# Optimization experiments

Hardware: AMD Instinct MI355X
Metric: run time of the kernel (lower is better)

Reference implementation:

```python
import jax, jax.numpy as jnp
import numpy as np
import math

N_HEAD = 16
V_HEAD = 32   # v_head_dim
NOPE = 32     # nope_head_dim
ROPE_D = 64   # rope_head_dim
KEEP = 256    # num_tokens_to_keep
EPS = 1e-6


def _freqs(T, dim=ROPE_D, theta=10000.0):
    f = 1.0 / (theta ** (jnp.arange(0, dim, 2, dtype=jnp.float32) / dim))
    t = jnp.arange(T, dtype=jnp.float32)
    a = jnp.outer(t, f)  # [T, dim//2]
    return jnp.cos(a), jnp.sin(a)


def _rope(x, cos, sin):
    # x: [B,H,S,D]; half-split rotation as in apply_rope
    S = x.shape[-2]
    c = cos[:S][None, None]
    s = sin[:S][None, None]
    x1, x2 = jnp.split(x, 2, axis=-1)
    return jnp.concatenate([x1 * c - x2 * s, x1 * s + x2 * c], axis=-1)


def _rms(x, g, eps=EPS):
    return x * jax.lax.rsqrt(jnp.mean(x * x, axis=-1, keepdims=True) + eps) * g


def _attn(q, k, v, causal):
    scale = 1.0 / math.sqrt(q.shape[-1])
    s = jnp.einsum('bhqd,bhkd->bhqk', q, k) * scale
    if causal:
        Tq, Tk = s.shape[-2], s.shape[-1]
        mask = jnp.tril(jnp.ones((Tq, Tk), dtype=bool))
        s = jnp.where(mask, s, jnp.finfo(s.dtype).min)
    return jnp.einsum('bhqk,bhkd->bhqd', jax.nn.softmax(s, axis=-1), v)


def _forward(x, w_cq, g_qnorm, w_dq_nope, w_dq_rope, w_ckv, g_kvnorm,
             w_dk_nope, w_dv, w_krope, w_imp, w_selk, w_selv,
             w_wink, w_winv, w_gate, w_proj):
    B, T, C = x.shape
    cos, sin = _freqs(T)

    # --- MLA query path ---
    nq = _rms(x @ w_cq, g_qnorm)                                  # [B,T,96]
    q_nope = (nq @ w_dq_nope).reshape(B, T, N_HEAD, NOPE).transpose(0, 2, 1, 3)
    q_rope = (nq @ w_dq_rope).reshape(B, T, N_HEAD, ROPE_D).transpose(0, 2, 1, 3)
    q_rope = _rope(q_rope, cos, sin)
    q = jnp.concatenate([q_nope, q_rope], axis=-1)                # [B,H,T,96]

    # --- branch gate ---
    gate = jax.nn.softmax((x @ w_gate).mean(axis=1), axis=-1)     # [B,3]

    # --- branch 1: MLA-compressed full KV ---
    ckv = _rms(x @ w_ckv, g_kvnorm)                               # [B,T,32]
    k_nope = (ckv @ w_dk_nope).reshape(B, T, N_HEAD, NOPE).transpose(0, 2, 1, 3)
    v1 = (ckv @ w_dv).reshape(B, T, N_HEAD, V_HEAD).transpose(0, 2, 1, 3)
    k_rope = (x @ w_krope).reshape(B, T, 1, ROPE_D).transpose(0, 2, 1, 3) / N_HEAD
    k_rope = _rope(k_rope, cos, sin)
    k1 = jnp.concatenate(
        [k_nope, jnp.broadcast_to(k_rope, (B, N_HEAD, T, ROPE_D))], axis=-1)

    # --- branch 2: top-k selected tokens ---
    scores = (x @ w_imp)[..., 0]                                  # [B,T]
    _, idx = jax.lax.top_k(scores, KEEP)
    idx = jnp.sort(idx, axis=1)
    sel = jnp.take_along_axis(x, idx[:, :, None], axis=1)         # [B,S,C]
    ks = (sel @ w_selk).reshape(B, KEEP, N_HEAD, NOPE + ROPE_D).transpose(0, 2, 1, 3)
    vs = (sel @ w_selv).reshape(B, KEEP, N_HEAD, V_HEAD).transpose(0, 2, 1, 3)
    ks = jnp.concatenate([ks[..., :NOPE], _rope(ks[..., NOPE:], cos, sin)], axis=-1)

    # --- branch 3: sliding window (training mode -> full x) ---
    kw = (x @ w_wink).reshape(B, T, N_HEAD, NOPE + ROPE_D).transpose(0, 2, 1, 3)
    vw = (x @ w_winv).reshape(B, T, N_HEAD, V_HEAD).transpose(0, 2, 1, 3)
    kw = jnp.concatenate([kw[..., :NOPE], _rope(kw[..., NOPE:], cos, sin)], axis=-1)

    a1 = _attn(q, k1, v1, causal=True)
    a2 = _attn(q, ks, vs, causal=False)
    a3 = _attn(q, kw, vw, causal=True)

    g = gate[:, :, None, None, None]
    out = g[:, 0] * a1 + g[:, 1] * a2 + g[:, 2] * a3              # [B,H,T,Vd]
    out = out.transpose(0, 2, 1, 3).reshape(B, T, N_HEAD * V_HEAD)
    return out @ w_proj                                           # [B,T,C]


def setup_inputs() -> dict:
    key = jax.random.key(0)
    ks = jax.random.split(key, 20)
    B, T, C = 2, 1024, 1024
    q_lora, kv_lora = 96, 32
    std = 0.02
    def w(k, shape):
        return jax.random.normal(k, shape, dtype=jnp.float32) * std
    return {
        'x': jax.random.normal(ks[0], (B, T, C), dtype=jnp.float32),
        'w_cq': w(ks[1], (C, q_lora)),
        'g_qnorm': jnp.ones((q_lora,), jnp.float32),
        'w_dq_nope': w(ks[2], (q_lora, N_HEAD * NOPE)),
        'w_dq_rope': w(ks[3], (q_lora, N_HEAD * ROPE_D)),
        'w_ckv': w(ks[4], (C, kv_lora)),
        'g_kvnorm': jnp.ones((kv_lora,), jnp.float32),
        'w_dk_nope': w(ks[5], (kv_lora, N_HEAD * NOPE)),
        'w_dv': w(ks[6], (kv_lora, N_HEAD * V_HEAD)),
        'w_krope': w(ks[7], (C, ROPE_D)),
        'w_imp': w(ks[8], (C, 1)),
        'w_selk': w(ks[9], (C, N_HEAD * (NOPE + ROPE_D))),
        'w_selv': w(ks[10], (C, N_HEAD * V_HEAD)),
        'w_wink': w(ks[11], (C, N_HEAD * (NOPE + ROPE_D))),
        'w_winv': w(ks[12], (C, N_HEAD * V_HEAD)),
        'w_gate': w(ks[13], (C, 3)),
        'w_proj': w(ks[14], (N_HEAD * V_HEAD, C)),
    }


def reference(x, w_cq, g_qnorm, w_dq_nope, w_dq_rope, w_ckv, g_kvnorm,
              w_dk_nope, w_dv, w_krope, w_imp, w_selk, w_selv,
              w_wink, w_winv, w_gate, w_proj):
    return _forward(x, w_cq, g_qnorm, w_dq_nope, w_dq_rope, w_ckv, g_kvnorm,
                    w_dk_nope, w_dv, w_krope, w_imp, w_selk, w_selv,
                    w_wink, w_winv, w_gate, w_proj)
```

## Files before the change

kernel.cpp:

```cpp
#include <hip/hip_runtime.h>
#include <math.h>

#define T_SEQ   1024
#define BATCH   2
#define CDIM    1024
#define NHEAD   16
#define VHEAD   32
#define KEEP    256
#define HEAD_D  96
#define SCALE_ATTN 0.1020620726159658f

#define BQ   64
#define BKT  64
#define SK   100
#define SPT  66
#define SPV  36

#define GBK 16
#define SA  132

#define XWW    2244
#define C_CQ   0
#define C_CKV  96
#define C_KRO  128
#define C_WINK 192
#define C_WINV 1728
#define C_IMP  2240
#define C_GATE 2241

#define QKVW   2560
#define C_QN   0
#define C_QR   512
#define C_KN   1536
#define C_V1   2048

#define SKW  2048

__global__ __launch_bounds__(256) void gemm128(const float* __restrict__ A,
                                               const float* __restrict__ B,
                                               float* __restrict__ C,
                                               int M, int N, int K,
                                               int lda, int ldb, int ldc,
                                               int kchunk) {
    __shared__ float As[GBK][SA];
    __shared__ float Bs[GBK][SA];
    int t = threadIdx.x;
    int tx = t & 15, ty = t >> 4;
    int row0 = blockIdx.y * 128, col0 = blockIdx.x * 128;
    int kb = blockIdx.z * kchunk;
    int ke = min(K, kb + kchunk);
    float acc[8][8] = {};

    for (int k0 = kb; k0 < ke; k0 += GBK) {
#pragma unroll
        for (int r = 0; r < 2; r++) {
            int idx = t + 256 * r;
            int row = idx >> 2, k4 = idx & 3;
            int gr = row0 + row;
            float4 v = make_float4(0.f, 0.f, 0.f, 0.f);
            if (gr < M) v = *(const float4*)&A[(size_t)gr * lda + k0 + k4 * 4];
            As[k4 * 4 + 0][row] = v.x;
            As[k4 * 4 + 1][row] = v.y;
            As[k4 * 4 + 2][row] = v.z;
            As[k4 * 4 + 3][row] = v.w;
        }
#pragma unroll
        for (int r = 0; r < 2; r++) {
            int idx = t + 256 * r;
            int kk = idx >> 5, n4 = idx & 31;
            int gc = col0 + n4 * 4;
            float4 v = make_float4(0.f, 0.f, 0.f, 0.f);
            if (gc + 3 < N) {
                v = *(const float4*)&B[(size_t)(k0 + kk) * ldb + gc];
            } else if (gc < N) {
                const float* bp = &B[(size_t)(k0 + kk) * ldb];
                float tmp[4] = {0.f, 0.f, 0.f, 0.f};
                for (int j = 0; j < 4 && gc + j < N; j++) tmp[j] = bp[gc + j];
                v = make_float4(tmp[0], tmp[1], tmp[2], tmp[3]);
            }
            *(float4*)&Bs[kk][n4 * 4] = v;
        }
        __syncthreads();
#pragma unroll
        for (int kk = 0; kk < GBK; kk++) {
            float4 a0 = *(float4*)&As[kk][ty * 4];
            float4 a1 = *(float4*)&As[kk][64 + ty * 4];
            float4 b0 = *(float4*)&Bs[kk][tx * 4];
            float4 b1 = *(float4*)&Bs[kk][64 + tx * 4];
            float av[8] = {a0.x, a0.y, a0.z, a0.w, a1.x, a1.y, a1.z, a1.w};
            float bv[8] = {b0.x, b0.y, b0.z, b0.w, b1.x, b1.y, b1.z, b1.w};
#pragma unroll
            for (int i = 0; i < 8; i++)
#pragma unroll
                for (int j = 0; j < 8; j++) acc[i][j] += av[i] * bv[j];
        }
        __syncthreads();
    }

    bool split = (gridDim.z > 1);
#pragma unroll
    for (int i = 0; i < 8; i++) {
        int gr = row0 + ((i < 4) ? (ty * 4 + i) : (64 + ty * 4 + (i - 4)));
        if (gr >= M) continue;
#pragma unroll
        for (int half = 0; half < 2; half++) {
            int gc = col0 + half * 64 + tx * 4;
            if (gc + 3 >= N) continue;
            float* cp = &C[(size_t)gr * ldc + gc];
            if (split) {
                atomicAdd(cp + 0, acc[i][half * 4 + 0]);
                atomicAdd(cp + 1, acc[i][half * 4 + 1]);
                atomicAdd(cp + 2, acc[i][half * 4 + 2]);
                atomicAdd(cp + 3, acc[i][half * 4 + 3]);
            } else {
                *(float4*)cp = make_float4(acc[i][half * 4 + 0], acc[i][half * 4 + 1],
                                           acc[i][half * 4 + 2], acc[i][half * 4 + 3]);
            }
        }
    }
}

__global__ void pack_xw(float* __restrict__ dst,
                        const float* __restrict__ cq, const float* __restrict__ ckv,
                        const float* __restrict__ kro, const float* __restrict__ wink,
                        const float* __restrict__ winv, const float* __restrict__ imp,
                        const float* __restrict__ gate) {
    int r = blockIdx.x;
    for (int c = threadIdx.x; c < XWW; c += blockDim.x) {
        float v;
        if      (c < C_CKV)  v = cq  [(size_t)r * 96   + c];
        else if (c < C_KRO)  v = ckv [(size_t)r * 32   + (c - C_CKV)];
        else if (c < C_WINK) v = kro [(size_t)r * 64   + (c - C_KRO)];
        else if (c < C_WINV) v = wink[(size_t)r * 1536 + (c - C_WINK)];
        else if (c < C_IMP)  v = winv[(size_t)r * 512  + (c - C_WINV)];
        else if (c < C_GATE) v = imp [(size_t)r * 1    + (c - C_IMP)];
        else                 v = gate[(size_t)r * 3    + (c - C_GATE)];
        dst[(size_t)r * XWW + c] = v;
    }
}

__global__ void pack_qkv(float* __restrict__ dst,
                         const float* __restrict__ dqn, const float* __restrict__ dqr,
                         const float* __restrict__ dkn, const float* __restrict__ dv) {
    int r = blockIdx.x;
    for (int c = threadIdx.x; c < QKVW; c += blockDim.x) {
        float v = 0.f;
        if (r < 96) {
            if (c < C_QR)      v = dqn[(size_t)r * 512 + c];
            else if (c < C_KN) v = dqr[(size_t)r * 1024 + (c - C_QR)];
        } else {
            if (c >= C_KN && c < C_V1) v = dkn[(size_t)(r - 96) * 512 + (c - C_KN)];
            else if (c >= C_V1)        v = dv [(size_t)(r - 96) * 512 + (c - C_V1)];
        }
        dst[(size_t)r * QKVW + c] = v;
    }
}

__global__ void pack2(float* __restrict__ dst,
                      const float* __restrict__ s0, int w0,
                      const float* __restrict__ s1, int w1) {
    int W = w0 + w1;
    int r = blockIdx.x;
    for (int c = threadIdx.x; c < W; c += blockDim.x) {
        float v = (c < w0) ? s0[(size_t)r * w0 + c] : s1[(size_t)r * w1 + (c - w0)];
        dst[(size_t)r * W + c] = v;
    }
}

__global__ void rms_rows(float* __restrict__ buf, const float* __restrict__ g,
                         int D, int stride) {
    int row = blockIdx.x;
    int lane = threadIdx.x;
    float* rp = buf + (size_t)row * stride;
    float ss = 0.f;
    for (int d = lane; d < D; d += 64) {
        float v = rp[d];
        ss += v * v;
    }
    for (int off = 32; off; off >>= 1) ss += __shfl_xor(ss, off, 64);
    float r = rsqrtf(ss / (float)D + 1e-6f);
    for (int d = lane; d < D; d += 64) rp[d] *= r * g[d];
}

__global__ void rope_inplace(float* __restrict__ buf, int nrows, int rstride,
                             int nheads, int hstride, int roff, int posmod,
                             float scale) {
    int total = nrows * nheads * 32;
    for (int it = blockIdx.x * blockDim.x + threadIdx.x; it < total;
         it += gridDim.x * blockDim.x) {
        int i = it & 31;
        int hr = it >> 5;
        int h = hr % nheads;
        int row = hr / nheads;
        int pos = row % posmod;
        float expo = (float)i * (1.0f / 32.0f);
        float f = 1.0f / powf(10000.0f, expo);
        float a = (float)pos * f;
        float s, c;
        sincosf(a, &s, &c);
        size_t base = (size_t)row * rstride + (size_t)h * hstride + roff;
        float v1 = buf[base + i], v2 = buf[base + 32 + i];
        buf[base + i]      = (v1 * c - v2 * s) * scale;
        buf[base + 32 + i] = (v1 * s + v2 * c) * scale;
    }
}

__global__ void gate_from_cols(const float* __restrict__ xw, float* __restrict__ gate) {
    int b = blockIdx.x;
    int t = threadIdx.x;
    __shared__ float red[3][4];
    float g0 = 0.f, g1 = 0.f, g2 = 0.f;
    for (int r = t; r < T_SEQ; r += 256) {
        const float* p = &xw[((size_t)b * T_SEQ + r) * XWW + C_GATE];
        g0 += p[0]; g1 += p[1]; g2 += p[2];
    }
    for (int off = 32; off; off >>= 1) {
        g0 += __shfl_xor(g0, off, 64);
        g1 += __shfl_xor(g1, off, 64);
        g2 += __shfl_xor(g2, off, 64);
    }
    int w = t >> 6;
    if ((t & 63) == 0) { red[0][w] = g0; red[1][w] = g1; red[2][w] = g2; }
    __syncthreads();
    if (t == 0) {
        float v0 = (red[0][0] + red[0][1] + red[0][2] + red[0][3]) / (float)T_SEQ;
        float v1 = (red[1][0] + red[1][1] + red[1][2] + red[1][3]) / (float)T_SEQ;
        float v2 = (red[2][0] + red[2][1] + red[2][2] + red[2][3]) / (float)T_SEQ;
        float m = fmaxf(v0, fmaxf(v1, v2));
        float e0 = expf(v0 - m), e1 = expf(v1 - m), e2 = expf(v2 - m);
        float s = e0 + e1 + e2;
        gate[b * 3 + 0] = e0 / s;
        gate[b * 3 + 1] = e1 / s;
        gate[b * 3 + 2] = e2 / s;
    }
}

__global__ void topk_kernel(const float* __restrict__ base, int stride, int col,
                            int* __restrict__ idx) {
    int b = blockIdx.x;
    __shared__ float s[1024];
    __shared__ int ps[1024];
    int t = threadIdx.x;
    s[t] = base[((size_t)b * T_SEQ + t) * stride + col];
    __syncthreads();
    float mine = s[t];
    int rank = 0;
    for (int j = 0; j < 1024; j++) {
        float v = s[j];
        rank += (v > mine) || (v == mine && j < t);
    }
    int selv = (rank < KEEP) ? 1 : 0;
    ps[t] = selv;
    __syncthreads();
    for (int off = 1; off < 1024; off <<= 1) {
        int add = (t >= off) ? ps[t - off] : 0;
        __syncthreads();
        ps[t] += add;
        __syncthreads();
    }
    if (selv) idx[b * KEEP + ps[t] - 1] = t;
}

__global__ void gather_sel(const float* __restrict__ x, const int* __restrict__ idx,
                           float* __restrict__ sel) {
    for (size_t i = (size_t)blockIdx.x * blockDim.x + threadIdx.x;
         i < (size_t)BATCH * KEEP * CDIM; i += (size_t)gridDim.x * blockDim.x) {
        int c = (int)(i & (CDIM - 1));
        int r = (int)((i >> 10) & (KEEP - 1));
        int b = (int)(i >> 18);
        sel[i] = x[((size_t)b * T_SEQ + idx[b * KEEP + r]) * CDIM + c];
    }
}

__global__ __launch_bounds__(512, 4) void flash_fused(
    const float* __restrict__ qkv, const float* __restrict__ xw,
    const float* __restrict__ skv, const float* __restrict__ gate,
    float* __restrict__ out) {
    __shared__ float Qs[BQ * SK];
    __shared__ float Ks[BKT * SK];
    __shared__ float Vs[BKT * SPV];
    __shared__ float Pt[BKT * SPT];

    int b = blockIdx.z, h = blockIdx.y;
    int qt = blockIdx.x;
    if (b == 1) qt = (gridDim.x - 1) - qt;
    int q0 = qt * BQ;
    int t = threadIdx.x;
    int tq = t >> 4, tk = t & 15;

    for (int i = t; i < BQ * 24; i += 512) {
        int row = i / 24, d4 = i % 24;
        size_t rq = (size_t)b * T_SEQ + q0 + row;
        float4 v;
        if (d4 < 8) v = *(const float4*)&qkv[rq * QKVW + C_QN + h * 32 + d4 * 4];
        else        v = *(const float4*)&qkv[rq * QKVW + C_QR + h * 64 + (d4 - 8) * 4];
        *(float4*)&Qs[row * SK + d4 * 4] = v;
    }

    int qq0 = q0 + 2 * tq, qq1 = qq0 + 1;
    float comb[2][2] = {};
    for (int phase = 0; phase < 3; phase++) {
        bool causal = (phase != 1);
        int ntiles = causal ? (qt + 1) : (KEEP / BKT);
        float m0 = -1e30f, m1 = -1e30f, l0 = 0.f, l1 = 0.f;
        float o00 = 0.f, o01 = 0.f, o10 = 0.f, o11 = 0.f;

        for (int kt = 0; kt < ntiles; kt++) {
            int j0 = kt * BKT;
            __syncthreads();

            for (int i = t; i < BKT * 24; i += 512) {
                int row = i / 24, d4 = i % 24;
                int j = j0 + row;
                float4 v;
                if (phase == 0) {
                    size_t rk = (size_t)b * T_SEQ + j;
                    if (d4 < 8) v = *(const float4*)&qkv[rk * QKVW + C_KN + h * 32 + d4 * 4];
                    else        v = *(const float4*)&xw[rk * XWW + C_KRO + (d4 - 8) * 4];
                } else if (phase == 1) {
                    v = *(const float4*)&skv[((size_t)b * KEEP + j) * SKW + h * 96 + d4 * 4];
                } else {
                    v = *(const float4*)&xw[((size_t)b * T_SEQ + j) * XWW + C_WINK + h * 96 + d4 * 4];
                }
                *(float4*)&Ks[row * SK + d4 * 4] = v;
            }
            for (int i = t; i < BKT * 8; i += 512) {
                int row = i >> 3, d4 = i & 7;
                int j = j0 + row;
                float4 v;
                if (phase == 0)      v = *(const float4*)&qkv[((size_t)b * T_SEQ + j) * QKVW + C_V1 + h * 32 + d4 * 4];
                else if (phase == 1) v = *(const float4*)&skv[((size_t)b * KEEP  + j) * SKW + 1536 + h * 32 + d4 * 4];
                else                 v = *(const float4*)&xw[((size_t)b * T_SEQ + j) * XWW + C_WINV + h * 32 + d4 * 4];
                *(float4*)&Vs[row * SPV + d4 * 4] = v;
            }
            __syncthreads();

            float s0[4] = {}, s1[4] = {};
#pragma unroll 6
            for (int d = 0; d < HEAD_D; d += 4) {
                float4 qa = *(float4*)&Qs[(2 * tq)     * SK + d];
                float4 qb = *(float4*)&Qs[(2 * tq + 1) * SK + d];
#pragma unroll
                for (int j = 0; j < 4; j++) {
                    float4 kv = *(float4*)&Ks[(16 * j + tk) * SK + d];
                    s0[j] += qa.x * kv.x + qa.y * kv.y + qa.z * kv.z + qa.w * kv.w;
                    s1[j] += qb.x * kv.x + qb.y * kv.y + qb.z * kv.z + qb.w * kv.w;
                }
            }
            float mt0 = -1e30f, mt1 = -1e30f;
#pragma unroll
            for (int j = 0; j < 4; j++) {
                int kk = j0 + 16 * j + tk;
                s0[j] *= SCALE_ATTN;
                s1[j] *= SCALE_ATTN;
                if (causal && kk > qq0) s0[j] = -1e30f;
                if (causal && kk > qq1) s1[j] = -1e30f;
                mt0 = fmaxf(mt0, s0[j]);
                mt1 = fmaxf(mt1, s1[j]);
            }
#pragma unroll
            for (int off = 1; off <= 8; off <<= 1) {
                mt0 = fmaxf(mt0, __shfl_xor(mt0, off, 64));
                mt1 = fmaxf(mt1, __shfl_xor(mt1, off, 64));
            }
            float mn0 = fmaxf(m0, mt0), mn1 = fmaxf(m1, mt1);
            float a0 = __expf(m0 - mn0), a1 = __expf(m1 - mn1);
            m0 = mn0; m1 = mn1;

            float rs0 = 0.f, rs1 = 0.f;
#pragma unroll
            for (int j = 0; j < 4; j++) {
                float p0 = __expf(s0[j] - mn0);
                float p1 = __expf(s1[j] - mn1);
                rs0 += p0; rs1 += p1;
                *(float2*)&Pt[(16 * j + tk) * SPT + 2 * tq] = make_float2(p0, p1);
            }
#pragma unroll
            for (int off = 1; off <= 8; off <<= 1) {
                rs0 += __shfl_xor(rs0, off, 64);
                rs1 += __shfl_xor(rs1, off, 64);
            }
            l0 = l0 * a0 + rs0;
            l1 = l1 * a1 + rs1;

            o00 *= a0; o01 *= a0; o10 *= a1; o11 *= a1;
#pragma unroll 8
            for (int kk = 0; kk < BKT; kk++) {
                float2 pv = *(float2*)&Pt[kk * SPT + 2 * tq];
                float2 vv = *(float2*)&Vs[kk * SPV + 2 * tk];
                o00 += pv.x * vv.x; o01 += pv.x * vv.y;
                o10 += pv.y * vv.x; o11 += pv.y * vv.y;
            }
        }

        float g = gate[b * 3 + phase];
        float i0 = g / l0, i1 = g / l1;
        comb[0][0] += o00 * i0; comb[0][1] += o01 * i0;
        comb[1][0] += o10 * i1; comb[1][1] += o11 * i1;
    }

    size_t r0 = ((size_t)b * T_SEQ + q0 + 2 * tq) * 512 + h * 32 + 2 * tk;
    out[r0]           = comb[0][0];
    out[r0 + 1]       = comb[0][1];
    out[r0 + 512]     = comb[1][0];
    out[r0 + 512 + 1] = comb[1][1];
}

extern "C" void kernel_launch(void* const* d_in, const int* in_sizes, int n_in,
                              void* d_out, int out_size, void* d_ws, size_t ws_size,
                              hipStream_t stream) {
    const float* x        = (const float*)d_in[0];
    const float* w_cq     = (const float*)d_in[1];
    const float* g_qnorm  = (const float*)d_in[2];
    const float* w_dqn    = (const float*)d_in[3];
    const float* w_dqr    = (const float*)d_in[4];
    const float* w_ckv    = (const float*)d_in[5];
    const float* g_kvnorm = (const float*)d_in[6];
    const float* w_dkn    = (const float*)d_in[7];
    const float* w_dv     = (const float*)d_in[8];
    const float* w_krope  = (const float*)d_in[9];
    const float* w_imp    = (const float*)d_in[10];
    const float* w_selk   = (const float*)d_in[11];
    const float* w_selv   = (const float*)d_in[12];
    const float* w_wink   = (const float*)d_in[13];
    const float* w_winv   = (const float*)d_in[14];
    const float* w_gate   = (const float*)d_in[15];
    const float* w_proj   = (const float*)d_in[16];
    float* out = (float*)d_out;

    const int BT = BATCH * T_SEQ;
    const int BS = BATCH * KEEP;

    float* ws = (float*)d_ws;
    size_t o = 0;
    float* XW     = ws + o; o += (size_t)BT * XWW;
    float* QKV    = ws + o; o += (size_t)BT * QKVW;
    float* skv    = ws + o; o += (size_t)BS * SKW;
    float* selb   = ws + o; o += (size_t)BS * CDIM;
    float* attn   = ws + o; o += (size_t)BT * 512;
    float* Bxw    = ws + o; o += (size_t)CDIM * XWW;
    float* Bqkv   = ws + o; o += (size_t)128 * QKVW;
    float* Bsel   = ws + o; o += (size_t)CDIM * SKW;
    float* gatef  = ws + o; o += 8;
    int*   idx    = (int*)(ws + o); o += 512;

    auto gemm = [&](const float* A, const float* Bm, float* C, int M, int N, int K,
                    int lda, int ldb, int ldc, int ksplit = 1) {
        int kchunk = (K / ksplit + GBK - 1) / GBK * GBK;
        dim3 grid((N + 127) / 128, (M + 127) / 128, ksplit);
        gemm128<<<grid, 256, 0, stream>>>(A, Bm, C, M, N, K, lda, ldb, ldc, kchunk);
    };

    hipMemsetAsync(skv, 0, (size_t)BS * SKW * sizeof(float), stream);
    hipMemsetAsync(out, 0, (size_t)BT * CDIM * sizeof(float), stream);

    pack_xw<<<1024, 256, 0, stream>>>(Bxw, w_cq, w_ckv, w_krope, w_wink, w_winv,
                                      w_imp, w_gate);
    pack_qkv<<<128, 256, 0, stream>>>(Bqkv, w_dqn, w_dqr, w_dkn, w_dv);
    pack2<<<1024, 256, 0, stream>>>(Bsel, w_selk, 1536, w_selv, 512);

    gemm(x, Bxw, XW, BT, XWW, CDIM, CDIM, XWW, XWW);

    rms_rows<<<BT, 64, 0, stream>>>(XW + C_CQ, g_qnorm, 96, XWW);
    rms_rows<<<BT, 64, 0, stream>>>(XW + C_CKV, g_kvnorm, 32, XWW);
    rope_inplace<<<256, 256, 0, stream>>>(XW, BT, XWW, 1, 0, C_KRO, T_SEQ, 1.0f / NHEAD);
    rope_inplace<<<2048, 256, 0, stream>>>(XW, BT, XWW, 16, 96, C_WINK + 32, T_SEQ, 1.0f);

    gate_from_cols<<<BATCH, 256, 0, stream>>>(XW, gatef);
    topk_kernel<<<BATCH, 1024, 0, stream>>>(XW, XWW, C_IMP, idx);
    gather_sel<<<2048, 256, 0, stream>>>(x, idx, selb);

    gemm(XW, Bqkv, QKV, BT, QKVW, 128, XWW, QKVW, QKVW);
    rope_inplace<<<2048, 256, 0, stream>>>(QKV, BT, QKVW, 16, 64, C_QR, T_SEQ, 1.0f);

    gemm(selb, Bsel, skv, BS, SKW, CDIM, CDIM, SKW, SKW, 4);
    rope_inplace<<<512, 256, 0, stream>>>(skv, BS, SKW, 16, 96, 32, KEEP, 1.0f);

    dim3 fgrid(T_SEQ / BQ, NHEAD, BATCH);
    flash_fused<<<fgrid, 512, 0, stream>>>(QKV, XW, skv, gatef, attn);

    gemm(attn, w_proj, out, BT, CDIM, 512, 512, CDIM, CDIM, 2);
}
```

Before: 978.7 us.

## Fuse pack, norm, rope and topk/gate kernels; precompute rope sin/cos table

Merges the three weight-pack kernels into one launch. It fuses the two RMS norms and two rope passes on the XW projection into a single per-row kernel, and folds the gate reduction into the top-k kernel. It also precomputes a cos/sin table once so the rope kernels read it instead of calling powf and sincosf per element. The aim is to cut launch count and repeated transcendental work; the small kernels are a minor share next to the GEMMs and the flash kernel.

Result: faster. 955.5 us (-2.4%).

```diff
diff --git a/kernel.cpp b/kernel.cpp
--- a/kernel.cpp
+++ b/kernel.cpp
@@ -120,71 +120,109 @@
     }
 }
 
-__global__ void pack_xw(float* __restrict__ dst,
-                        const float* __restrict__ cq, const float* __restrict__ ckv,
-                        const float* __restrict__ kro, const float* __restrict__ wink,
-                        const float* __restrict__ winv, const float* __restrict__ imp,
-                        const float* __restrict__ gate) {
-    int r = blockIdx.x;
-    for (int c = threadIdx.x; c < XWW; c += blockDim.x) {
-        float v;
-        if      (c < C_CKV)  v = cq  [(size_t)r * 96   + c];
-        else if (c < C_KRO)  v = ckv [(size_t)r * 32   + (c - C_CKV)];
-        else if (c < C_WINK) v = kro [(size_t)r * 64   + (c - C_KRO)];
-        else if (c < C_WINV) v = wink[(size_t)r * 1536 + (c - C_WINK)];
-        else if (c < C_IMP)  v = winv[(size_t)r * 512  + (c - C_WINV)];
-        else if (c < C_GATE) v = imp [(size_t)r * 1    + (c - C_IMP)];
-        else                 v = gate[(size_t)r * 3    + (c - C_GATE)];
-        dst[(size_t)r * XWW + c] = v;
-    }
-}
-
-__global__ void pack_qkv(float* __restrict__ dst,
+__global__ void build_tab(float2* __restrict__ tab) {
+    int idx = blockIdx.x * blockDim.x + threadIdx.x;
+    if (idx >= T_SEQ * 32) return;
+    int pos = idx >> 5, i = idx & 31;
+    float expo = (float)i * (1.0f / 32.0f);
+    float f = 1.0f / powf(10000.0f, expo);
+    float a = (float)pos * f;
+    float s, c;
+    sincosf(a, &s, &c);
+    tab[idx] = make_float2(c, s);
+}
+
+__global__ void pack_all(float* __restrict__ Bxw, float* __restrict__ Bqkv,
+                         float* __restrict__ Bsel,
+                         const float* __restrict__ cq, const float* __restrict__ ckv,
+                         const float* __restrict__ kro, const float* __restrict__ wink,
+                         const float* __restrict__ winv, const float* __restrict__ imp,
+                         const float* __restrict__ gate,
                          const float* __restrict__ dqn, const float* __restrict__ dqr,
-                         const float* __restrict__ dkn, const float* __restrict__ dv) {
-    int r = blockIdx.x;
-    for (int c = threadIdx.x; c < QKVW; c += blockDim.x) {
-        float v = 0.f;
-        if (r < 96) {
-            if (c < C_QR)      v = dqn[(size_t)r * 512 + c];
-            else if (c < C_KN) v = dqr[(size_t)r * 1024 + (c - C_QR)];
-        } else {
-            if (c >= C_KN && c < C_V1) v = dkn[(size_t)(r - 96) * 512 + (c - C_KN)];
-            else if (c >= C_V1)        v = dv [(size_t)(r - 96) * 512 + (c - C_V1)];
-        }
-        dst[(size_t)r * QKVW + c] = v;
-    }
-}
-
-__global__ void pack2(float* __restrict__ dst,
-                      const float* __restrict__ s0, int w0,
-                      const float* __restrict__ s1, int w1) {
-    int W = w0 + w1;
-    int r = blockIdx.x;
-    for (int c = threadIdx.x; c < W; c += blockDim.x) {
-        float v = (c < w0) ? s0[(size_t)r * w0 + c] : s1[(size_t)r * w1 + (c - w0)];
-        dst[(size_t)r * W + c] = v;
-    }
-}
-
-__global__ void rms_rows(float* __restrict__ buf, const float* __restrict__ g,
-                         int D, int stride) {
+                         const float* __restrict__ dkn, const float* __restrict__ dv,
+                         const float* __restrict__ selk, const float* __restrict__ selv) {
+    int blk = blockIdx.x;
+    if (blk < 1024) {
+        int r = blk;
+        for (int c = threadIdx.x; c < XWW; c += blockDim.x) {
+            float v;
+            if      (c < C_CKV)  v = cq  [(size_t)r * 96   + c];
+            else if (c < C_KRO)  v = ckv [(size_t)r * 32   + (c - C_CKV)];
+            else if (c < C_WINK) v = kro [(size_t)r * 64   + (c - C_KRO)];
+            else if (c < C_WINV) v = wink[(size_t)r * 1536 + (c - C_WINK)];
+            else if (c < C_IMP)  v = winv[(size_t)r * 512  + (c - C_WINV)];
+            else if (c < C_GATE) v = imp [(size_t)r * 1    + (c - C_IMP)];
+            else                 v = gate[(size_t)r * 3    + (c - C_GATE)];
+            Bxw[(size_t)r * XWW + c] = v;
+        }
+    } else if (blk < 1152) {
+        int r = blk - 1024;
+        for (int c = threadIdx.x; c < QKVW; c += blockDim.x) {
+            float v = 0.f;
+            if (r < 96) {
+                if (c < C_QR)      v = dqn[(size_t)r * 512 + c];
+                else if (c < C_KN) v = dqr[(size_t)r * 1024 + (c - C_QR)];
+            } else {
+                if (c >= C_KN && c < C_V1) v = dkn[(size_t)(r - 96) * 512 + (c - C_KN)];
+                else if (c >= C_V1)        v = dv [(size_t)(r - 96) * 512 + (c - C_V1)];
+            }
+            Bqkv[(size_t)r * QKVW + c] = v;
+        }
+    } else {
+        int r = blk - 1152;
+        for (int c = threadIdx.x; c < SKW; c += blockDim.x) {
+            float v = (c < 1536) ? selk[(size_t)r * 1536 + c]
+                                 : selv[(size_t)r * 512 + (c - 1536)];
+            Bsel[(size_t)r * SKW + c] = v;
+        }
+    }
+}
+
+__global__ void xw_post(float* __restrict__ XW, const float* __restrict__ gq,
+                        const float* __restrict__ gkv,
+                        const float2* __restrict__ tab) {
     int row = blockIdx.x;
-    int lane = threadIdx.x;
-    float* rp = buf + (size_t)row * stride;
-    float ss = 0.f;
-    for (int d = lane; d < D; d += 64) {
-        float v = rp[d];
-        ss += v * v;
-    }
-    for (int off = 32; off; off >>= 1) ss += __shfl_xor(ss, off, 64);
-    float r = rsqrtf(ss / (float)D + 1e-6f);
-    for (int d = lane; d < D; d += 64) rp[d] *= r * g[d];
-}
-
-__global__ void rope_inplace(float* __restrict__ buf, int nrows, int rstride,
-                             int nheads, int hstride, int roff, int posmod,
-                             float scale) {
+    int t = threadIdx.x;
+    int w = t >> 6, lane = t & 63;
+    float* rp = XW + (size_t)row * XWW;
+    int pos = row & (T_SEQ - 1);
+    const float2* tp = tab + pos * 32;
+
+    if (w == 0) {
+        float ss = 0.f;
+        for (int d = lane; d < 96; d += 64) { float v = rp[d]; ss += v * v; }
+        for (int off = 32; off; off >>= 1) ss += __shfl_xor(ss, off, 64);
+        float r = rsqrtf(ss / 96.0f + 1e-6f);
+        for (int d = lane; d < 96; d += 64) rp[d] *= r * gq[d];
+    } else if (w == 1) {
+        float ss = 0.f;
+        for (int d = lane; d < 32; d += 64) { float v = rp[C_CKV + d]; ss += v * v; }
+        for (int off = 32; off; off >>= 1) ss += __shfl_xor(ss, off, 64);
+        float r = rsqrtf(ss / 32.0f + 1e-6f);
+        for (int d = lane; d < 32; d += 64) rp[C_CKV + d] *= r * gkv[d];
+    } else if (w == 2) {
+        if (lane < 32) {
+            float2 cs = tp[lane];
+            float v1 = rp[C_KRO + lane], v2 = rp[C_KRO + 32 + lane];
+            rp[C_KRO + lane]      = (v1 * cs.x - v2 * cs.y) * (1.0f / NHEAD);
+            rp[C_KRO + 32 + lane] = (v1 * cs.y + v2 * cs.x) * (1.0f / NHEAD);
+        }
+    }
+#pragma unroll
+    for (int j = 0; j < 2; j++) {
+        int item = t + j * 256;
+        int h = item >> 5, i = item & 31;
+        float2 cs = tp[i];
+        size_t base = (size_t)(C_WINK + 32) + h * 96;
+        float v1 = rp[base + i], v2 = rp[base + 32 + i];
+        rp[base + i]      = v1 * cs.x - v2 * cs.y;
+        rp[base + 32 + i] = v1 * cs.y + v2 * cs.x;
+    }
+}
+
+__global__ void rope_tab(float* __restrict__ buf, int nrows, int rstride,
+                         int nheads, int hstride, int roff, int posmod,
+                         const float2* __restrict__ tab) {
     int total = nrows * nheads * 32;
     for (int it = blockIdx.x * blockDim.x + threadIdx.x; it < total;
          it += gridDim.x * blockDim.x) {
@@ -193,55 +231,42 @@
         int h = hr % nheads;
         int row = hr / nheads;
         int pos = row % posmod;
-        float expo = (float)i * (1.0f / 32.0f);
-        float f = 1.0f / powf(10000.0f, expo);
-        float a = (float)pos * f;
-        float s, c;
-        sincosf(a, &s, &c);
+        float2 cs = tab[pos * 32 + i];
         size_t base = (size_t)row * rstride + (size_t)h * hstride + roff;
         float v1 = buf[base + i], v2 = buf[base + 32 + i];
-        buf[base + i]      = (v1 * c - v2 * s) * scale;
-        buf[base + 32 + i] = (v1 * s + v2 * c) * scale;
-    }
-}
-
-__global__ void gate_from_cols(const float* __restrict__ xw, float* __restrict__ gate) {
+        buf[base + i]      = v1 * cs.x - v2 * cs.y;
+        buf[base + 32 + i] = v1 * cs.y + v2 * cs.x;
+    }
+}
+
+__global__ void topk_gate(const float* __restrict__ xw, int* __restrict__ idx,
+                          float* __restrict__ gate) {
     int b = blockIdx.x;
+    __shared__ float s[1024];
+    __shared__ int ps[1024];
+    __shared__ float gred[3][16];
     int t = threadIdx.x;
-    __shared__ float red[3][4];
-    float g0 = 0.f, g1 = 0.f, g2 = 0.f;
-    for (int r = t; r < T_SEQ; r += 256) {
-        const float* p = &xw[((size_t)b * T_SEQ + r) * XWW + C_GATE];
-        g0 += p[0]; g1 += p[1]; g2 += p[2];
-    }
+    const float* rowp = &xw[((size_t)b * T_SEQ + t) * XWW];
+    s[t] = rowp[C_IMP];
+    float g0 = rowp[C_GATE + 0], g1 = rowp[C_GATE + 1], g2 = rowp[C_GATE + 2];
     for (int off = 32; off; off >>= 1) {
         g0 += __shfl_xor(g0, off, 64);
         g1 += __shfl_xor(g1, off, 64);
         g2 += __shfl_xor(g2, off, 64);
     }
-    int w = t >> 6;
-    if ((t & 63) == 0) { red[0][w] = g0; red[1][w] = g1; red[2][w] = g2; }
+    if ((t & 63) == 0) { int w = t >> 6; gred[0][w] = g0; gred[1][w] = g1; gred[2][w] = g2; }
     __syncthreads();
     if (t == 0) {
-        float v0 = (red[0][0] + red[0][1] + red[0][2] + red[0][3]) / (float)T_SEQ;
-        float v1 = (red[1][0] + red[1][1] + red[1][2] + red[1][3]) / (float)T_SEQ;
-        float v2 = (red[2][0] + red[2][1] + red[2][2] + red[2][3]) / (float)T_SEQ;
+        float v0 = 0.f, v1 = 0.f, v2 = 0.f;
+        for (int w = 0; w < 16; w++) { v0 += gred[0][w]; v1 += gred[1][w]; v2 += gred[2][w]; }
+        v0 /= (float)T_SEQ; v1 /= (float)T_SEQ; v2 /= (float)T_SEQ;
         float m = fmaxf(v0, fmaxf(v1, v2));
         float e0 = expf(v0 - m), e1 = expf(v1 - m), e2 = expf(v2 - m);
-        float s = e0 + e1 + e2;
-        gate[b * 3 + 0] = e0 / s;
-        gate[b * 3 + 1] = e1 / s;
-        gate[b * 3 + 2] = e2 / s;
-    }
-}
-
-__global__ void topk_kernel(const float* __restrict__ base, int stride, int col,
-                            int* __restrict__ idx) {
-    int b = blockIdx.x;
-    __shared__ float s[1024];
-    __shared__ int ps[1024];
-    int t = threadIdx.x;
-    s[t] = base[((size_t)b * T_SEQ + t) * stride + col];
+        float ssum = e0 + e1 + e2;
+        gate[b * 3 + 0] = e0 / ssum;
+        gate[b * 3 + 1] = e1 / ssum;
+        gate[b * 3 + 2] = e2 / ssum;
+    }
     __syncthreads();
     float mine = s[t];
     int rank = 0;
@@ -441,6 +466,7 @@
     float* Bxw    = ws + o; o += (size_t)CDIM * XWW;
     float* Bqkv   = ws + o; o += (size_t)128 * QKVW;
     float* Bsel   = ws + o; o += (size_t)CDIM * SKW;
+    float2* tab   = (float2*)(ws + o); o += (size_t)T_SEQ * 32 * 2;
     float* gatef  = ws + o; o += 8;
     int*   idx    = (int*)(ws + o); o += 512;
 
@@ -454,27 +480,24 @@
     hipMemsetAsync(skv, 0, (size_t)BS * SKW * sizeof(float), stream);
     hipMemsetAsync(out, 0, (size_t)BT * CDIM * sizeof(float), stream);
 
-    pack_xw<<<1024, 256, 0, stream>>>(Bxw, w_cq, w_ckv, w_krope, w_wink, w_winv,
-                                      w_imp, w_gate);
-    pack_qkv<<<128, 256, 0, stream>>>(Bqkv, w_dqn, w_dqr, w_dkn, w_dv);
-    pack2<<<1024, 256, 0, stream>>>(Bsel, w_selk, 1536, w_selv, 512);
+    pack_all<<<2176, 256, 0, stream>>>(Bxw, Bqkv, Bsel,
+                                       w_cq, w_ckv, w_krope, w_wink, w_winv,
+                                       w_imp, w_gate,
+                                       w_dqn, w_dqr, w_dkn, w_dv, w_selk, w_selv);
+    build_tab<<<64, 512, 0, stream>>>(tab);
 
     gemm(x, Bxw, XW, BT, XWW, CDIM, CDIM, XWW, XWW);
 
-    rms_rows<<<BT, 64, 0, stream>>>(XW + C_CQ, g_qnorm, 96, XWW);
-    rms_rows<<<BT, 64, 0, stream>>>(XW + C_CKV, g_kvnorm, 32, XWW);
-    rope_inplace<<<256, 256, 0, stream>>>(XW, BT, XWW, 1, 0, C_KRO, T_SEQ, 1.0f / NHEAD);
-    rope_inplace<<<2048, 256, 0, stream>>>(XW, BT, XWW, 16, 96, C_WINK + 32, T_SEQ, 1.0f);
-
-    gate_from_cols<<<BATCH, 256, 0, stream>>>(XW, gatef);
-    topk_kernel<<<BATCH, 1024, 0, stream>>>(XW, XWW, C_IMP, idx);
+    xw_post<<<BT, 256, 0, stream>>>(XW, g_qnorm, g_kvnorm, tab);
+
+    topk_gate<<<BATCH, 1024, 0, stream>>>(XW, idx, gatef);
     gather_sel<<<2048, 256, 0, stream>>>(x, idx, selb);
 
     gemm(XW, Bqkv, QKV, BT, QKVW, 128, XWW, QKVW, QKVW);
-    rope_inplace<<<2048, 256, 0, stream>>>(QKV, BT, QKVW, 16, 64, C_QR, T_SEQ, 1.0f);
+    rope_tab<<<2048, 256, 0, stream>>>(QKV, BT, QKVW, 16, 64, C_QR, T_SEQ, tab);
 
     gemm(selb, Bsel, skv, BS, SKW, CDIM, CDIM, SKW, SKW, 4);
-    rope_inplace<<<512, 256, 0, stream>>>(skv, BS, SKW, 16, 96, 32, KEEP, 1.0f);
+    rope_tab<<<512, 256, 0, stream>>>(skv, BS, SKW, 16, 96, 32, KEEP, tab);
 
     dim3 fgrid(T_SEQ / BQ, NHEAD, BATCH);
     flash_fused<<<fgrid, 512, 0, stream>>>(QKV, XW, skv, gatef, attn);
```
